# Optimization experiments

Measured on AMD Instinct MI355X. Metric: run time of the kernel, lower is better.

Reference implementation:

```python
import jax, jax.numpy as jnp
import numpy as np

CODEBOOK_SIZE = 1024
CODEBOOK_DIM = 256
B, H, W = 32, 64, 64


def setup_inputs() -> dict:
    key = jax.random.key(0)
    kx, kc = jax.random.split(key)
    x = jax.random.normal(kx, (B, CODEBOOK_DIM, H, W), dtype=jnp.float32)
    # nn.init.uniform_(weight, -1/K, 1/K)
    bound = 1.0 / CODEBOOK_SIZE
    codebook = jax.random.uniform(kc, (CODEBOOK_SIZE, CODEBOOK_DIM),
                                  minval=-bound, maxval=bound, dtype=jnp.float32)
    return {"x": x, "codebook": codebook}


def reference(x, codebook):
    b, c, h, w = x.shape
    z_e = jnp.transpose(x, (0, 2, 3, 1))            # [b,h,w,c]
    z_flat = z_e.reshape(-1, c)                      # [N,c]
    # squared L2 distances: ||z||^2 + ||e||^2 - 2 z.e
    dists = (jnp.sum(z_flat * z_flat, axis=1, keepdims=True)
             + jnp.sum(codebook * codebook, axis=1)
             - 2.0 * jnp.matmul(z_flat, codebook.T))  # [N,K]
    idx = jnp.argmin(dists, axis=1)                  # [N] int
    z_q = codebook[idx].reshape(b, h, w, c)          # [b,h,w,c]
    # commitment + codebook loss (both detach patterns)
    loss = (jnp.mean((jax.lax.stop_gradient(z_e) - z_q) ** 2)
            + jnp.mean((jax.lax.stop_gradient(z_q) - z_e) ** 2))
    # straight-through estimator
    z_q_st = z_e + jax.lax.stop_gradient(z_q - z_e)
    z_q_out = jnp.transpose(z_q_st, (0, 3, 1, 2))    # [b,c,h,w]
    return z_q_out, idx, loss
```

## Files before the change

kernel.cpp:

```cpp
#include <hip/hip_runtime.h>


typedef __attribute__((ext_vector_type(8))) short short8;
typedef __attribute__((ext_vector_type(4))) float f32x4;
typedef unsigned long long u64;

#define IDX_OFF   33554432u
#define LOSS_OFF  33685504u
#define IMG_BYTE  67108864u
#define CAND_BYTE 68157440u
#define ENRM_BYTE 69206016u

__device__ __forceinline__ unsigned short f2bf(float f) {
  unsigned u = __float_as_uint(f);
  unsigned r = (u + 0x7FFFu + ((u >> 16) & 1u)) >> 16;
  return (unsigned short)r;
}

#define COMB(r) __fadd_rn(__fadd_rn(__fadd_rn(r[0], r[1]), __fadd_rn(r[2], r[3])), \
                          __fadd_rn(__fadd_rn(r[4], r[5]), __fadd_rn(r[6], r[7])))

extern "C" __global__ __launch_bounds__(256) void vq_r11_k0(const float* __restrict__ cb,
                                                            unsigned char* __restrict__ img,
                                                            float* __restrict__ outf) {
  unsigned tid = blockIdx.x * 256u + threadIdx.x;
  unsigned code = tid >> 7, dp = tid & 127u;
  const float* p = cb + (size_t)code * 256u + dp * 2u;
  unsigned u = ((unsigned)f2bf(p[1]) << 16) | (unsigned)f2bf(p[0]);
  unsigned kc = code >> 6, n = (code >> 4) & 3, c16 = code & 15;
  unsigned ks = dp >> 4, g = (dp >> 2) & 3, j = dp & 3;
  unsigned byte = kc * 32768u + (n * 8u + ks) * 1024u + (g * 16u + c16) * 16u + j * 4u;
  *(unsigned*)(img + byte) = u;
  if (tid == 0) outf[LOSS_OFF] = 0.0f;
}

extern "C" __global__ __launch_bounds__(256) void vq_r11_k0b(const float* __restrict__ cb,
                                                             float* __restrict__ enrm) {
#pragma clang fp contract(off)
  int c = blockIdx.x * 256 + threadIdx.x;
  const float* e = cb + (size_t)c * 256u;
  float h[2];
#pragma unroll
  for (int half = 0; half < 2; ++half) {
    float r[8];
#pragma unroll
    for (int j = 0; j < 8; ++j) {
      float v = e[half * 128 + j];
      r[j] = __fmul_rn(v, v);
    }
    for (int i = 8; i < 128; i += 8) {
#pragma unroll
      for (int j = 0; j < 8; ++j) {
        float v = e[half * 128 + i + j];
        r[j] = __fadd_rn(r[j], __fmul_rn(v, v));
      }
    }
    h[half] = COMB(r);
  }
  enrm[c] = __fadd_rn(h[0], h[1]);
}

__device__ __forceinline__ void issue_frags(const unsigned char* gsrc, char* ldst) {
#pragma unroll
  for (int ks = 0; ks < 8; ++ks)
    __builtin_amdgcn_global_load_lds(
        (const __attribute__((address_space(1))) unsigned int*)(gsrc + ks * 1024),
        (__attribute__((address_space(3))) unsigned int*)(ldst + ks * 1024),
        16, 0, 0);
}

extern "C" __global__ __launch_bounds__(256, 2) void vq_r11_k1(const float* __restrict__ x,
                                                               const unsigned char* __restrict__ img,
                                                               u64* __restrict__ cand4) {
  __shared__ __attribute__((aligned(16))) char lds[65536];
  const int t = threadIdx.x;
  const int bid = blockIdx.x;
  const int lane = t & 63;
  const int w = t >> 6;
  const int g = lane >> 4, c16 = lane & 15;

  const size_t xbase = (size_t)(bid >> 4) * 1048576u + (size_t)(bid & 15) * 256u;

  short8 a[4][8];
  for (int q = 0; q < 4; ++q) {
#pragma unroll 4
    for (int s = 0; s < 8; ++s) {
      int flat = s * 256 + t;
      int pt4 = flat & 15;
      int dp = flat >> 4;
      const float* px = x + xbase + (size_t)(2 * dp) * 4096u + (unsigned)(q * 64 + pt4 * 4);
      float4 fa = *(const float4*)px;
      float4 fb = *(const float4*)(px + 4096);
      const float* fap = (const float*)&fa;
      const float* fbp = (const float*)&fb;
#pragma unroll
      for (int k = 0; k < 4; ++k) {
        unsigned u = ((unsigned)f2bf(fbp[k]) << 16) | (unsigned)f2bf(fap[k]);
        int r = pt4 * 4 + k;
        *(unsigned*)(lds + r * 512 + ((dp * 4) ^ ((r & 31) << 2))) = u;
      }
    }
    __syncthreads();
    if (w == q) {
#pragma unroll
      for (int m = 0; m < 4; ++m) {
        const int r = m * 16 + c16;
        const int rsw = (r & 31) << 2;
#pragma unroll
        for (int ks = 0; ks < 8; ++ks) {
          union { unsigned q4[4]; short8 s8; } uu;
#pragma unroll
          for (int jj = 0; jj < 4; ++jj)
            uu.q4[jj] = *(const unsigned*)(lds + r * 512 + (((ks * 16 + g * 4 + jj) * 4) ^ rsw));
          a[m][ks] = uu.s8;
        }
      }
    }
    __syncthreads();
  }

  float t1[16], t2[16];
#pragma unroll
  for (int s = 0; s < 16; ++s) { t1[s] = -__builtin_inff(); t2[s] = -__builtin_inff(); }

  char* ldsW = lds + w * 16384;
  const unsigned char* gW = img + (unsigned)(lane * 16);

  issue_frags(gW, ldsW);

  for (int s = 0; s < 64; ++s) {
    char* cur = ldsW + (s & 1) * 8192;
    asm volatile("s_waitcnt lgkmcnt(0)" ::: "memory");
    if (s < 63) {
      issue_frags(gW + (unsigned)((s + 1) * 8192), ldsW + ((s + 1) & 1) * 8192);
      asm volatile("s_waitcnt vmcnt(8)" ::: "memory");
    } else {
      asm volatile("s_waitcnt vmcnt(0)" ::: "memory");
    }

    f32x4 acc0 = (f32x4){0.f, 0.f, 0.f, 0.f};
    f32x4 acc1 = (f32x4){0.f, 0.f, 0.f, 0.f};
    f32x4 acc2 = (f32x4){0.f, 0.f, 0.f, 0.f};
    f32x4 acc3 = (f32x4){0.f, 0.f, 0.f, 0.f};
#pragma unroll
    for (int ks = 0; ks < 8; ++ks) {
      short8 b = *(const short8*)(cur + ks * 1024 + lane * 16);
      acc0 = __builtin_amdgcn_mfma_f32_16x16x32_bf16(a[0][ks], b, acc0, 0, 0, 0);
      acc1 = __builtin_amdgcn_mfma_f32_16x16x32_bf16(a[1][ks], b, acc1, 0, 0, 0);
      acc2 = __builtin_amdgcn_mfma_f32_16x16x32_bf16(a[2][ks], b, acc2, 0, 0, 0);
      acc3 = __builtin_amdgcn_mfma_f32_16x16x32_bf16(a[3][ks], b, acc3, 0, 0, 0);
    }
    const unsigned code = (unsigned)(s * 16 + c16);
#define SCRN(v, sl) { float kf = __uint_as_float((__float_as_uint(v) & 0xFFFFFC00u) | code); \
                      t2[sl] = __builtin_amdgcn_fmed3f(kf, t1[sl], t2[sl]); \
                      t1[sl] = fmaxf(t1[sl], kf); }
#pragma unroll
    for (int i = 0; i < 4; ++i) {
      SCRN(acc0[i], i);
      SCRN(acc1[i], 4 + i);
      SCRN(acc2[i], 8 + i);
      SCRN(acc3[i], 12 + i);
    }
#undef SCRN
  }

  __syncthreads();
  float* kk = (float*)lds;
#pragma unroll
  for (int m = 0; m < 4; ++m)
#pragma unroll
    for (int i = 0; i < 4; ++i) {
      int pt = w * 64 + m * 16 + g * 4 + i;
      kk[pt * 32 + c16 * 2] = t1[m * 4 + i];
      kk[pt * 32 + c16 * 2 + 1] = t2[m * 4 + i];
    }
  __syncthreads();

  {
    float f1 = -__builtin_inff(), f2v = f1, f3 = f1, f4 = f1;
#pragma unroll
    for (int j = 0; j < 32; ++j) {
      float v = kk[t * 32 + ((j + t) & 31)];
      float b1 = fminf(f1, v);   f1 = fmaxf(f1, v);
      float b2 = fminf(f2v, b1); f2v = fmaxf(f2v, b1);
      float b3 = fminf(f3, b2);  f3 = fmaxf(f3, b2);
      f4 = fmaxf(f4, b3);
    }
    u64 pk = (u64)(__float_as_uint(f1) & 1023u)
           | ((u64)(__float_as_uint(f2v) & 1023u) << 16)
           | ((u64)(__float_as_uint(f3) & 1023u) << 32)
           | ((u64)(__float_as_uint(f4) & 1023u) << 48);
    cand4[(size_t)bid * 256u + (unsigned)t] = pk;
  }
}

extern "C" __global__ __launch_bounds__(256) void vq_r11_k2(const float* __restrict__ x,
                                                            const float* __restrict__ cb,
                                                            const u64* __restrict__ cand4,
                                                            const float* __restrict__ enrm,
                                                            float* __restrict__ outf) {
#pragma clang fp contract(off)
  __shared__ double dts[4][64];
  __shared__ float s1s[64];
  const int t = threadIdx.x;
  const int pl = t & 63;
  const int c = t >> 6;
  const unsigned p = blockIdx.x * 64u + (unsigned)pl;

  const u64 pk = cand4[p];
  const int code = (int)((pk >> (16 * c)) & 1023u);

  const size_t xoff = ((size_t)(p >> 12)) * 1048576u + (size_t)(p & 4095u);
  const float* e = cb + (size_t)code * 256u;

  double da = 0.0, db = 0.0;
  float hs1[2];
#pragma unroll
  for (int half = 0; half < 2; ++half) {
    float r[8];
#pragma unroll 2
    for (int i = 0; i < 128; i += 8) {
      const int dbase = half * 128 + i;
      float q[8], xv[8];
      *(float4*)(q) = *(const float4*)(e + dbase);
      *(float4*)(q + 4) = *(const float4*)(e + dbase + 4);
#pragma unroll
      for (int j = 0; j < 8; ++j) xv[j] = x[xoff + (size_t)(dbase + j) * 4096u];
#pragma unroll
      for (int j = 0; j < 8; ++j) {
        r[j] = (i == 0) ? __fmul_rn(xv[j], xv[j])
                        : __fadd_rn(r[j], __fmul_rn(xv[j], xv[j]));
        if (j & 1) db = fma((double)xv[j], (double)q[j], db);
        else       da = fma((double)xv[j], (double)q[j], da);
      }
    }
    hs1[half] = COMB(r);
  }
  dts[c][pl] = da + db;
  if (c == 0) s1s[pl] = __fadd_rn(hs1[0], hs1[1]);
  __syncthreads();

  if (t < 64) {
    const float s1v = s1s[pl];
    float bestd = __builtin_inff();
    int besti = 0x7FFFFFFF;
#pragma unroll
    for (int cc = 0; cc < 4; ++cc) {
      const int ccode = (int)((pk >> (16 * cc)) & 1023u);
      float dd = __fsub_rn(__fadd_rn(s1v, enrm[ccode]),
                           __fmul_rn(2.0f, (float)dts[cc][pl]));
      if (dd < bestd || (dd == bestd && ccode < besti)) { bestd = dd; besti = ccode; }
    }
    outf[IDX_OFF + p] = (float)besti;

    float sum = bestd;
#pragma unroll
    for (int off = 32; off > 0; off >>= 1) sum += __shfl_down(sum, off);
    if (pl == 0) atomicAdd(outf + LOSS_OFF, sum);
  }
}

extern "C" __global__ void vq_r11_k4(float* __restrict__ outf) {
  if (threadIdx.x == 0 && blockIdx.x == 0)
    outf[LOSS_OFF] = 2.0f * (outf[LOSS_OFF] / 33554432.0f);
}

extern "C" __global__ __launch_bounds__(256) void vq_r11_k3(const float* __restrict__ cb,
                                                            float* __restrict__ outf) {
  __shared__ float rows[32 * 257];
  const int t = threadIdx.x;
  const unsigned p0 = blockIdx.x * 32u;
  const unsigned b = p0 >> 12, hw0 = p0 & 4095u;
  const float* idxf = outf + IDX_OFF;
  for (int i = 0; i < 32; ++i) {
    int row = ((int)idxf[p0 + (unsigned)i]) & 1023;
    rows[i * 257 + t] = cb[(size_t)row * 256u + (unsigned)t];
  }
  __syncthreads();
  const int q = t & 7, cgrp = t >> 3;
  float* obase = outf + (size_t)b * 1048576u + hw0 + (unsigned)(q * 4);
#pragma unroll
  for (int cc = 0; cc < 8; ++cc) {
    int c = cgrp * 8 + cc;
    float4 v;
    v.x = rows[(q * 4 + 0) * 257 + c];
    v.y = rows[(q * 4 + 1) * 257 + c];
    v.z = rows[(q * 4 + 2) * 257 + c];
    v.w = rows[(q * 4 + 3) * 257 + c];
    *(float4*)(obase + (size_t)c * 4096u) = v;
  }
}

extern "C" void kernel_launch(void* const* d_in, const int* in_sizes, int n_in,
                              void* d_out, int out_size, void* d_ws, size_t ws_size,
                              hipStream_t stream) {
  const float* x = (const float*)d_in[0];
  const float* cb = (const float*)d_in[1];
  float* outf = (float*)d_out;
  unsigned char* img = (unsigned char*)d_out + IMG_BYTE;
  u64* cand4 = (u64*)((unsigned char*)d_out + CAND_BYTE);
  float* enrm = (float*)((unsigned char*)d_out + ENRM_BYTE);
  (void)in_sizes; (void)n_in; (void)out_size; (void)d_ws; (void)ws_size;

  vq_r11_k0<<<512, 256, 0, stream>>>(cb, img, outf);
  vq_r11_k0b<<<4, 256, 0, stream>>>(cb, enrm);
  vq_r11_k1<<<512, 256, 0, stream>>>(x, img, cand4);
  vq_r11_k2<<<2048, 256, 0, stream>>>(x, cb, cand4, enrm, outf);
  vq_r11_k4<<<1, 64, 0, stream>>>(outf);
  vq_r11_k3<<<4096, 256, 0, stream>>>(cb, outf);
}
```

Before: 214.2 us.

## Load codebook fragments directly into registers and ping-pong accumulators across steps

The distance kernel stops staging codebook fragments through LDS with global_load_lds double buffering. It now loads the B fragments straight from global memory into registers. The codebook image layout is simplified to one contiguous 8 KB block per 16-code step, and the main loop is unrolled by two with alternating accumulator sets so the top-2 screening of one step overlaps the MFMAs and loads of the next. LDS shrinks to 32 KB, used only by the A-tile transpose and the final merge. The trade-off is higher register pressure and exposed global-load latency instead of LDS staging.

```diff
diff --git a/kernel.cpp b/kernel.cpp
--- a/kernel.cpp
+++ b/kernel.cpp
@@ -20,21 +20,21 @@
 #define COMB(r) __fadd_rn(__fadd_rn(__fadd_rn(r[0], r[1]), __fadd_rn(r[2], r[3])), \
                           __fadd_rn(__fadd_rn(r[4], r[5]), __fadd_rn(r[6], r[7])))
 
-extern "C" __global__ __launch_bounds__(256) void vq_r11_k0(const float* __restrict__ cb,
+extern "C" __global__ __launch_bounds__(256) void vq_r12_k0(const float* __restrict__ cb,
                                                             unsigned char* __restrict__ img,
                                                             float* __restrict__ outf) {
   unsigned tid = blockIdx.x * 256u + threadIdx.x;
   unsigned code = tid >> 7, dp = tid & 127u;
   const float* p = cb + (size_t)code * 256u + dp * 2u;
   unsigned u = ((unsigned)f2bf(p[1]) << 16) | (unsigned)f2bf(p[0]);
-  unsigned kc = code >> 6, n = (code >> 4) & 3, c16 = code & 15;
+  unsigned s = code >> 4, c16 = code & 15;
   unsigned ks = dp >> 4, g = (dp >> 2) & 3, j = dp & 3;
-  unsigned byte = kc * 32768u + (n * 8u + ks) * 1024u + (g * 16u + c16) * 16u + j * 4u;
+  unsigned byte = (s * 8u + ks) * 1024u + (g * 16u + c16) * 16u + j * 4u;
   *(unsigned*)(img + byte) = u;
   if (tid == 0) outf[LOSS_OFF] = 0.0f;
 }
 
-extern "C" __global__ __launch_bounds__(256) void vq_r11_k0b(const float* __restrict__ cb,
+extern "C" __global__ __launch_bounds__(256) void vq_r12_k0b(const float* __restrict__ cb,
                                                              float* __restrict__ enrm) {
 #pragma clang fp contract(off)
   int c = blockIdx.x * 256 + threadIdx.x;
@@ -60,19 +60,23 @@
   enrm[c] = __fadd_rn(h[0], h[1]);
 }
 
-__device__ __forceinline__ void issue_frags(const unsigned char* gsrc, char* ldst) {
-#pragma unroll
-  for (int ks = 0; ks < 8; ++ks)
-    __builtin_amdgcn_global_load_lds(
-        (const __attribute__((address_space(1))) unsigned int*)(gsrc + ks * 1024),
-        (__attribute__((address_space(3))) unsigned int*)(ldst + ks * 1024),
-        16, 0, 0);
-}
-
-extern "C" __global__ __launch_bounds__(256, 2) void vq_r11_k1(const float* __restrict__ x,
+__device__ __forceinline__ void screen16(const f32x4* acc, unsigned code,
+                                         float* t1, float* t2) {
+#pragma unroll
+  for (int m = 0; m < 4; ++m)
+#pragma unroll
+    for (int i = 0; i < 4; ++i) {
+      float kf = __uint_as_float((__float_as_uint(acc[m][i]) & 0xFFFFFC00u) | code);
+      int s = m * 4 + i;
+      t2[s] = __builtin_amdgcn_fmed3f(kf, t1[s], t2[s]);
+      t1[s] = fmaxf(t1[s], kf);
+    }
+}
+
+extern "C" __global__ __launch_bounds__(256, 2) void vq_r12_k1(const float* __restrict__ x,
                                                                const unsigned char* __restrict__ img,
                                                                u64* __restrict__ cand4) {
-  __shared__ __attribute__((aligned(16))) char lds[65536];
+  __shared__ __attribute__((aligned(16))) char lds[32768];
   const int t = threadIdx.x;
   const int bid = blockIdx.x;
   const int lane = t & 63;
@@ -123,48 +127,51 @@
 #pragma unroll
   for (int s = 0; s < 16; ++s) { t1[s] = -__builtin_inff(); t2[s] = -__builtin_inff(); }
 
-  char* ldsW = lds + w * 16384;
   const unsigned char* gW = img + (unsigned)(lane * 16);
-
-  issue_frags(gW, ldsW);
-
-  for (int s = 0; s < 64; ++s) {
-    char* cur = ldsW + (s & 1) * 8192;
-    asm volatile("s_waitcnt lgkmcnt(0)" ::: "memory");
-    if (s < 63) {
-      issue_frags(gW + (unsigned)((s + 1) * 8192), ldsW + ((s + 1) & 1) * 8192);
-      asm volatile("s_waitcnt vmcnt(8)" ::: "memory");
-    } else {
-      asm volatile("s_waitcnt vmcnt(0)" ::: "memory");
-    }
-
-    f32x4 acc0 = (f32x4){0.f, 0.f, 0.f, 0.f};
-    f32x4 acc1 = (f32x4){0.f, 0.f, 0.f, 0.f};
-    f32x4 acc2 = (f32x4){0.f, 0.f, 0.f, 0.f};
-    f32x4 acc3 = (f32x4){0.f, 0.f, 0.f, 0.f};
+  short8 bf[8];
+  f32x4 accA[4], accB[4];
+
+#pragma unroll
+  for (int ks = 0; ks < 8; ++ks)
+    bf[ks] = *(const short8*)(gW + ks * 1024);
+
+  for (int s2 = 0; s2 < 32; ++s2) {
+    const int s = s2 * 2;
+#pragma unroll
+    for (int i = 0; i < 4; ++i) accA[i] = (f32x4){0.f, 0.f, 0.f, 0.f};
 #pragma unroll
     for (int ks = 0; ks < 8; ++ks) {
-      short8 b = *(const short8*)(cur + ks * 1024 + lane * 16);
-      acc0 = __builtin_amdgcn_mfma_f32_16x16x32_bf16(a[0][ks], b, acc0, 0, 0, 0);
-      acc1 = __builtin_amdgcn_mfma_f32_16x16x32_bf16(a[1][ks], b, acc1, 0, 0, 0);
-      acc2 = __builtin_amdgcn_mfma_f32_16x16x32_bf16(a[2][ks], b, acc2, 0, 0, 0);
-      acc3 = __builtin_amdgcn_mfma_f32_16x16x32_bf16(a[3][ks], b, acc3, 0, 0, 0);
-    }
-    const unsigned code = (unsigned)(s * 16 + c16);
-#define SCRN(v, sl) { float kf = __uint_as_float((__float_as_uint(v) & 0xFFFFFC00u) | code); \
-                      t2[sl] = __builtin_amdgcn_fmed3f(kf, t1[sl], t2[sl]); \
-                      t1[sl] = fmaxf(t1[sl], kf); }
-#pragma unroll
-    for (int i = 0; i < 4; ++i) {
-      SCRN(acc0[i], i);
-      SCRN(acc1[i], 4 + i);
-      SCRN(acc2[i], 8 + i);
-      SCRN(acc3[i], 12 + i);
-    }
-#undef SCRN
-  }
-
-  __syncthreads();
+      accA[0] = __builtin_amdgcn_mfma_f32_16x16x32_bf16(a[0][ks], bf[ks], accA[0], 0, 0, 0);
+      accA[1] = __builtin_amdgcn_mfma_f32_16x16x32_bf16(a[1][ks], bf[ks], accA[1], 0, 0, 0);
+      accA[2] = __builtin_amdgcn_mfma_f32_16x16x32_bf16(a[2][ks], bf[ks], accA[2], 0, 0, 0);
+      accA[3] = __builtin_amdgcn_mfma_f32_16x16x32_bf16(a[3][ks], bf[ks], accA[3], 0, 0, 0);
+    }
+    {
+      const unsigned char* g1 = gW + (unsigned)((s + 1) * 8192);
+#pragma unroll
+      for (int ks = 0; ks < 8; ++ks) bf[ks] = *(const short8*)(g1 + ks * 1024);
+    }
+    if (s2 != 0)
+      screen16(accB, (unsigned)((s - 1) * 16 + c16), t1, t2);
+
+#pragma unroll
+    for (int i = 0; i < 4; ++i) accB[i] = (f32x4){0.f, 0.f, 0.f, 0.f};
+#pragma unroll
+    for (int ks = 0; ks < 8; ++ks) {
+      accB[0] = __builtin_amdgcn_mfma_f32_16x16x32_bf16(a[0][ks], bf[ks], accB[0], 0, 0, 0);
+      accB[1] = __builtin_amdgcn_mfma_f32_16x16x32_bf16(a[1][ks], bf[ks], accB[1], 0, 0, 0);
+      accB[2] = __builtin_amdgcn_mfma_f32_16x16x32_bf16(a[2][ks], bf[ks], accB[2], 0, 0, 0);
+      accB[3] = __builtin_amdgcn_mfma_f32_16x16x32_bf16(a[3][ks], bf[ks], accB[3], 0, 0, 0);
+    }
+    if (s2 != 31) {
+      const unsigned char* g2 = gW + (unsigned)((s + 2) * 8192);
+#pragma unroll
+      for (int ks = 0; ks < 8; ++ks) bf[ks] = *(const short8*)(g2 + ks * 1024);
+    }
+    screen16(accA, (unsigned)(s * 16 + c16), t1, t2);
+  }
+  screen16(accB, (unsigned)(63 * 16 + c16), t1, t2);
+
   float* kk = (float*)lds;
 #pragma unroll
   for (int m = 0; m < 4; ++m)
@@ -194,7 +201,7 @@
   }
 }
 
-extern "C" __global__ __launch_bounds__(256) void vq_r11_k2(const float* __restrict__ x,
+extern "C" __global__ __launch_bounds__(256) void vq_r12_k2(const float* __restrict__ x,
                                                             const float* __restrict__ cb,
                                                             const u64* __restrict__ cand4,
                                                             const float* __restrict__ enrm,
@@ -260,12 +267,12 @@
   }
 }
 
-extern "C" __global__ void vq_r11_k4(float* __restrict__ outf) {
+extern "C" __global__ void vq_r12_k4(float* __restrict__ outf) {
   if (threadIdx.x == 0 && blockIdx.x == 0)
     outf[LOSS_OFF] = 2.0f * (outf[LOSS_OFF] / 33554432.0f);
 }
 
-extern "C" __global__ __launch_bounds__(256) void vq_r11_k3(const float* __restrict__ cb,
+extern "C" __global__ __launch_bounds__(256) void vq_r12_k3(const float* __restrict__ cb,
                                                             float* __restrict__ outf) {
   __shared__ float rows[32 * 257];
   const int t = threadIdx.x;
@@ -302,10 +309,10 @@
   float* enrm = (float*)((unsigned char*)d_out + ENRM_BYTE);
   (void)in_sizes; (void)n_in; (void)out_size; (void)d_ws; (void)ws_size;
 
-  vq_r11_k0<<<512, 256, 0, stream>>>(cb, img, outf);
-  vq_r11_k0b<<<4, 256, 0, stream>>>(cb, enrm);
-  vq_r11_k1<<<512, 256, 0, stream>>>(x, img, cand4);
-  vq_r11_k2<<<2048, 256, 0, stream>>>(x, cb, cand4, enrm, outf);
-  vq_r11_k4<<<1, 64, 0, stream>>>(outf);
-  vq_r11_k3<<<4096, 256, 0, stream>>>(cb, outf);
-}
+  vq_r12_k0<<<512, 256, 0, stream>>>(cb, img, outf);
+  vq_r12_k0b<<<4, 256, 0, stream>>>(cb, enrm);
+  vq_r12_k1<<<512, 256, 0, stream>>>(x, img, cand4);
+  vq_r12_k2<<<2048, 256, 0, stream>>>(x, cb, cand4, enrm, outf);
+  vq_r12_k4<<<1, 64, 0, stream>>>(outf);
+  vq_r12_k3<<<4096, 256, 0, stream>>>(cb, outf);
+}
```

New measurement: 212.3 us. Within noise of the previous version (-0.9%).

## Halve points per block, load codebook fragments directly to registers, raise occupancy

Applied to the files above, without the earlier changes.

The distance kernel now handles 128 points per block instead of 256, and each wave holds 32 query rows instead of 64. The global→LDS double-buffered prefetch of codebook tiles is replaced by direct global loads into registers, with the codebook image relaid out linearly by code group. LDS drops to 32KB, launch bounds allow 3 blocks per CU, and the grid doubles to 1024. The intent is more occupancy and less LDS traffic, at the cost of reading the codebook twice as often in total and having less MFMA work per loaded B fragment.

```diff
diff --git a/kernel.cpp b/kernel.cpp
--- a/kernel.cpp
+++ b/kernel.cpp
@@ -20,21 +20,21 @@
 #define COMB(r) __fadd_rn(__fadd_rn(__fadd_rn(r[0], r[1]), __fadd_rn(r[2], r[3])), \
                           __fadd_rn(__fadd_rn(r[4], r[5]), __fadd_rn(r[6], r[7])))
 
-extern "C" __global__ __launch_bounds__(256) void vq_r11_k0(const float* __restrict__ cb,
+extern "C" __global__ __launch_bounds__(256) void vq_r13_k0(const float* __restrict__ cb,
                                                             unsigned char* __restrict__ img,
                                                             float* __restrict__ outf) {
   unsigned tid = blockIdx.x * 256u + threadIdx.x;
   unsigned code = tid >> 7, dp = tid & 127u;
   const float* p = cb + (size_t)code * 256u + dp * 2u;
   unsigned u = ((unsigned)f2bf(p[1]) << 16) | (unsigned)f2bf(p[0]);
-  unsigned kc = code >> 6, n = (code >> 4) & 3, c16 = code & 15;
+  unsigned s = code >> 4, c16 = code & 15;
   unsigned ks = dp >> 4, g = (dp >> 2) & 3, j = dp & 3;
-  unsigned byte = kc * 32768u + (n * 8u + ks) * 1024u + (g * 16u + c16) * 16u + j * 4u;
+  unsigned byte = (s * 8u + ks) * 1024u + (g * 16u + c16) * 16u + j * 4u;
   *(unsigned*)(img + byte) = u;
   if (tid == 0) outf[LOSS_OFF] = 0.0f;
 }
 
-extern "C" __global__ __launch_bounds__(256) void vq_r11_k0b(const float* __restrict__ cb,
+extern "C" __global__ __launch_bounds__(256) void vq_r13_k0b(const float* __restrict__ cb,
                                                              float* __restrict__ enrm) {
 #pragma clang fp contract(off)
   int c = blockIdx.x * 256 + threadIdx.x;
@@ -60,35 +60,26 @@
   enrm[c] = __fadd_rn(h[0], h[1]);
 }
 
-__device__ __forceinline__ void issue_frags(const unsigned char* gsrc, char* ldst) {
-#pragma unroll
-  for (int ks = 0; ks < 8; ++ks)
-    __builtin_amdgcn_global_load_lds(
-        (const __attribute__((address_space(1))) unsigned int*)(gsrc + ks * 1024),
-        (__attribute__((address_space(3))) unsigned int*)(ldst + ks * 1024),
-        16, 0, 0);
-}
-
-extern "C" __global__ __launch_bounds__(256, 2) void vq_r11_k1(const float* __restrict__ x,
+extern "C" __global__ __launch_bounds__(256, 3) void vq_r13_k1(const float* __restrict__ x,
                                                                const unsigned char* __restrict__ img,
                                                                u64* __restrict__ cand4) {
-  __shared__ __attribute__((aligned(16))) char lds[65536];
+  __shared__ __attribute__((aligned(16))) char lds[32768];
   const int t = threadIdx.x;
   const int bid = blockIdx.x;
   const int lane = t & 63;
   const int w = t >> 6;
   const int g = lane >> 4, c16 = lane & 15;
 
-  const size_t xbase = (size_t)(bid >> 4) * 1048576u + (size_t)(bid & 15) * 256u;
-
-  short8 a[4][8];
-  for (int q = 0; q < 4; ++q) {
+  const size_t xbase = (size_t)(bid >> 5) * 1048576u + (size_t)(bid & 31) * 128u;
+
+  short8 a[2][8];
+  for (int h = 0; h < 2; ++h) {
 #pragma unroll 4
-    for (int s = 0; s < 8; ++s) {
-      int flat = s * 256 + t;
+    for (int it = 0; it < 8; ++it) {
+      int flat = it * 256 + t;
       int pt4 = flat & 15;
       int dp = flat >> 4;
-      const float* px = x + xbase + (size_t)(2 * dp) * 4096u + (unsigned)(q * 64 + pt4 * 4);
+      const float* px = x + xbase + (size_t)(2 * dp) * 4096u + (unsigned)(h * 64 + pt4 * 4);
       float4 fa = *(const float4*)px;
       float4 fb = *(const float4*)(px + 4096);
       const float* fap = (const float*)&fa;
@@ -101,10 +92,10 @@
       }
     }
     __syncthreads();
-    if (w == q) {
-#pragma unroll
-      for (int m = 0; m < 4; ++m) {
-        const int r = m * 16 + c16;
+    if ((w >> 1) == h) {
+#pragma unroll
+      for (int m = 0; m < 2; ++m) {
+        const int r = (w & 1) * 32 + m * 16 + c16;
         const int rsw = (r & 31) << 2;
 #pragma unroll
         for (int ks = 0; ks < 8; ++ks) {
@@ -119,36 +110,23 @@
     __syncthreads();
   }
 
-  float t1[16], t2[16];
-#pragma unroll
-  for (int s = 0; s < 16; ++s) { t1[s] = -__builtin_inff(); t2[s] = -__builtin_inff(); }
-
-  char* ldsW = lds + w * 16384;
+  float t1[8], t2[8];
+#pragma unroll
+  for (int s = 0; s < 8; ++s) { t1[s] = -__builtin_inff(); t2[s] = -__builtin_inff(); }
+
   const unsigned char* gW = img + (unsigned)(lane * 16);
-
-  issue_frags(gW, ldsW);
-
   for (int s = 0; s < 64; ++s) {
-    char* cur = ldsW + (s & 1) * 8192;
-    asm volatile("s_waitcnt lgkmcnt(0)" ::: "memory");
-    if (s < 63) {
-      issue_frags(gW + (unsigned)((s + 1) * 8192), ldsW + ((s + 1) & 1) * 8192);
-      asm volatile("s_waitcnt vmcnt(8)" ::: "memory");
-    } else {
-      asm volatile("s_waitcnt vmcnt(0)" ::: "memory");
-    }
-
+    const unsigned char* gs = gW + (unsigned)(s * 8192);
+    short8 bf[8];
+#pragma unroll
+    for (int ks = 0; ks < 8; ++ks)
+      bf[ks] = *(const short8*)(gs + ks * 1024);
     f32x4 acc0 = (f32x4){0.f, 0.f, 0.f, 0.f};
     f32x4 acc1 = (f32x4){0.f, 0.f, 0.f, 0.f};
-    f32x4 acc2 = (f32x4){0.f, 0.f, 0.f, 0.f};
-    f32x4 acc3 = (f32x4){0.f, 0.f, 0.f, 0.f};
 #pragma unroll
     for (int ks = 0; ks < 8; ++ks) {
-      short8 b = *(const short8*)(cur + ks * 1024 + lane * 16);
-      acc0 = __builtin_amdgcn_mfma_f32_16x16x32_bf16(a[0][ks], b, acc0, 0, 0, 0);
-      acc1 = __builtin_amdgcn_mfma_f32_16x16x32_bf16(a[1][ks], b, acc1, 0, 0, 0);
-      acc2 = __builtin_amdgcn_mfma_f32_16x16x32_bf16(a[2][ks], b, acc2, 0, 0, 0);
-      acc3 = __builtin_amdgcn_mfma_f32_16x16x32_bf16(a[3][ks], b, acc3, 0, 0, 0);
+      acc0 = __builtin_amdgcn_mfma_f32_16x16x32_bf16(a[0][ks], bf[ks], acc0, 0, 0, 0);
+      acc1 = __builtin_amdgcn_mfma_f32_16x16x32_bf16(a[1][ks], bf[ks], acc1, 0, 0, 0);
     }
     const unsigned code = (unsigned)(s * 16 + c16);
 #define SCRN(v, sl) { float kf = __uint_as_float((__float_as_uint(v) & 0xFFFFFC00u) | code); \
@@ -158,8 +136,6 @@
     for (int i = 0; i < 4; ++i) {
       SCRN(acc0[i], i);
       SCRN(acc1[i], 4 + i);
-      SCRN(acc2[i], 8 + i);
-      SCRN(acc3[i], 12 + i);
     }
 #undef SCRN
   }
@@ -167,16 +143,16 @@
   __syncthreads();
   float* kk = (float*)lds;
 #pragma unroll
-  for (int m = 0; m < 4; ++m)
+  for (int m = 0; m < 2; ++m)
 #pragma unroll
     for (int i = 0; i < 4; ++i) {
-      int pt = w * 64 + m * 16 + g * 4 + i;
+      int pt = w * 32 + m * 16 + g * 4 + i;
       kk[pt * 32 + c16 * 2] = t1[m * 4 + i];
       kk[pt * 32 + c16 * 2 + 1] = t2[m * 4 + i];
     }
   __syncthreads();
 
-  {
+  if (t < 128) {
     float f1 = -__builtin_inff(), f2v = f1, f3 = f1, f4 = f1;
 #pragma unroll
     for (int j = 0; j < 32; ++j) {
@@ -190,11 +166,11 @@
            | ((u64)(__float_as_uint(f2v) & 1023u) << 16)
            | ((u64)(__float_as_uint(f3) & 1023u) << 32)
            | ((u64)(__float_as_uint(f4) & 1023u) << 48);
-    cand4[(size_t)bid * 256u + (unsigned)t] = pk;
-  }
-}
-
-extern "C" __global__ __launch_bounds__(256) void vq_r11_k2(const float* __restrict__ x,
+    cand4[(size_t)bid * 128u + (unsigned)t] = pk;
+  }
+}
+
+extern "C" __global__ __launch_bounds__(256) void vq_r13_k2(const float* __restrict__ x,
                                                             const float* __restrict__ cb,
                                                             const u64* __restrict__ cand4,
                                                             const float* __restrict__ enrm,
@@ -260,12 +236,12 @@
   }
 }
 
-extern "C" __global__ void vq_r11_k4(float* __restrict__ outf) {
+extern "C" __global__ void vq_r13_k4(float* __restrict__ outf) {
   if (threadIdx.x == 0 && blockIdx.x == 0)
     outf[LOSS_OFF] = 2.0f * (outf[LOSS_OFF] / 33554432.0f);
 }
 
-extern "C" __global__ __launch_bounds__(256) void vq_r11_k3(const float* __restrict__ cb,
+extern "C" __global__ __launch_bounds__(256) void vq_r13_k3(const float* __restrict__ cb,
                                                             float* __restrict__ outf) {
   __shared__ float rows[32 * 257];
   const int t = threadIdx.x;
@@ -302,10 +278,10 @@
   float* enrm = (float*)((unsigned char*)d_out + ENRM_BYTE);
   (void)in_sizes; (void)n_in; (void)out_size; (void)d_ws; (void)ws_size;
 
-  vq_r11_k0<<<512, 256, 0, stream>>>(cb, img, outf);
-  vq_r11_k0b<<<4, 256, 0, stream>>>(cb, enrm);
-  vq_r11_k1<<<512, 256, 0, stream>>>(x, img, cand4);
-  vq_r11_k2<<<2048, 256, 0, stream>>>(x, cb, cand4, enrm, outf);
-  vq_r11_k4<<<1, 64, 0, stream>>>(outf);
-  vq_r11_k3<<<4096, 256, 0, stream>>>(cb, outf);
-}
+  vq_r13_k0<<<512, 256, 0, stream>>>(cb, img, outf);
+  vq_r13_k0b<<<4, 256, 0, stream>>>(cb, enrm);
+  vq_r13_k1<<<1024, 256, 0, stream>>>(x, img, cand4);
+  vq_r13_k2<<<2048, 256, 0, stream>>>(x, cb, cand4, enrm, outf);
+  vq_r13_k4<<<1, 64, 0, stream>>>(outf);
+  vq_r13_k3<<<4096, 256, 0, stream>>>(cb, outf);
+}
```

Result: slower. 223.2 us (+4.2%).

## Load codebook fragments directly to registers and fold small kernels together

Applied to the files above, without the earlier changes.

The main scoring kernel no longer stages codebook B-fragments through double-buffered LDS with async global_load_lds. It reads them straight from global memory into registers each step, raises wave priority around the MFMA block, and halves the LDS allocation, which may allow more occupancy. The codebook-norm kernel is merged into the bf16 image-packing kernel, and the loss-finalize kernel is folded into the gather kernel, removing two launches. The image layout is simplified to match the new per-step read pattern. The trade-off is that global load latency is no longer overlapped by an explicit prefetch. The loss finalization in block 0 of the gather kernel relies on stream ordering after the accumulating kernel.

```diff
diff --git a/kernel.cpp b/kernel.cpp
--- a/kernel.cpp
+++ b/kernel.cpp
@@ -20,59 +20,49 @@
 #define COMB(r) __fadd_rn(__fadd_rn(__fadd_rn(r[0], r[1]), __fadd_rn(r[2], r[3])), \
                           __fadd_rn(__fadd_rn(r[4], r[5]), __fadd_rn(r[6], r[7])))
 
-extern "C" __global__ __launch_bounds__(256) void vq_r11_k0(const float* __restrict__ cb,
+extern "C" __global__ __launch_bounds__(256) void vq_r14_k0(const float* __restrict__ cb,
                                                             unsigned char* __restrict__ img,
+                                                            float* __restrict__ enrm,
                                                             float* __restrict__ outf) {
+#pragma clang fp contract(off)
   unsigned tid = blockIdx.x * 256u + threadIdx.x;
   unsigned code = tid >> 7, dp = tid & 127u;
   const float* p = cb + (size_t)code * 256u + dp * 2u;
   unsigned u = ((unsigned)f2bf(p[1]) << 16) | (unsigned)f2bf(p[0]);
-  unsigned kc = code >> 6, n = (code >> 4) & 3, c16 = code & 15;
+  unsigned s = code >> 4, c16 = code & 15;
   unsigned ks = dp >> 4, g = (dp >> 2) & 3, j = dp & 3;
-  unsigned byte = kc * 32768u + (n * 8u + ks) * 1024u + (g * 16u + c16) * 16u + j * 4u;
+  unsigned byte = (s * 8u + ks) * 1024u + (g * 16u + c16) * 16u + j * 4u;
   *(unsigned*)(img + byte) = u;
   if (tid == 0) outf[LOSS_OFF] = 0.0f;
-}
-
-extern "C" __global__ __launch_bounds__(256) void vq_r11_k0b(const float* __restrict__ cb,
-                                                             float* __restrict__ enrm) {
-#pragma clang fp contract(off)
-  int c = blockIdx.x * 256 + threadIdx.x;
-  const float* e = cb + (size_t)c * 256u;
-  float h[2];
-#pragma unroll
-  for (int half = 0; half < 2; ++half) {
-    float r[8];
-#pragma unroll
-    for (int j = 0; j < 8; ++j) {
-      float v = e[half * 128 + j];
-      r[j] = __fmul_rn(v, v);
-    }
-    for (int i = 8; i < 128; i += 8) {
-#pragma unroll
-      for (int j = 0; j < 8; ++j) {
-        float v = e[half * 128 + i + j];
-        r[j] = __fadd_rn(r[j], __fmul_rn(v, v));
-      }
-    }
-    h[half] = COMB(r);
-  }
-  enrm[c] = __fadd_rn(h[0], h[1]);
-}
-
-__device__ __forceinline__ void issue_frags(const unsigned char* gsrc, char* ldst) {
-#pragma unroll
-  for (int ks = 0; ks < 8; ++ks)
-    __builtin_amdgcn_global_load_lds(
-        (const __attribute__((address_space(1))) unsigned int*)(gsrc + ks * 1024),
-        (__attribute__((address_space(3))) unsigned int*)(ldst + ks * 1024),
-        16, 0, 0);
-}
-
-extern "C" __global__ __launch_bounds__(256, 2) void vq_r11_k1(const float* __restrict__ x,
+
+  if (tid < 1024u) {
+    const float* e = cb + (size_t)tid * 256u;
+    float h[2];
+#pragma unroll
+    for (int half = 0; half < 2; ++half) {
+      float r[8];
+#pragma unroll
+      for (int jj = 0; jj < 8; ++jj) {
+        float v = e[half * 128 + jj];
+        r[jj] = __fmul_rn(v, v);
+      }
+      for (int i = 8; i < 128; i += 8) {
+#pragma unroll
+        for (int jj = 0; jj < 8; ++jj) {
+          float v = e[half * 128 + i + jj];
+          r[jj] = __fadd_rn(r[jj], __fmul_rn(v, v));
+        }
+      }
+      h[half] = COMB(r);
+    }
+    enrm[tid] = __fadd_rn(h[0], h[1]);
+  }
+}
+
+extern "C" __global__ __launch_bounds__(256, 2) void vq_r14_k1(const float* __restrict__ x,
                                                                const unsigned char* __restrict__ img,
                                                                u64* __restrict__ cand4) {
-  __shared__ __attribute__((aligned(16))) char lds[65536];
+  __shared__ __attribute__((aligned(16))) char lds[32768];
   const int t = threadIdx.x;
   const int bid = blockIdx.x;
   const int lane = t & 63;
@@ -123,33 +113,26 @@
 #pragma unroll
   for (int s = 0; s < 16; ++s) { t1[s] = -__builtin_inff(); t2[s] = -__builtin_inff(); }
 
-  char* ldsW = lds + w * 16384;
   const unsigned char* gW = img + (unsigned)(lane * 16);
-
-  issue_frags(gW, ldsW);
-
   for (int s = 0; s < 64; ++s) {
-    char* cur = ldsW + (s & 1) * 8192;
-    asm volatile("s_waitcnt lgkmcnt(0)" ::: "memory");
-    if (s < 63) {
-      issue_frags(gW + (unsigned)((s + 1) * 8192), ldsW + ((s + 1) & 1) * 8192);
-      asm volatile("s_waitcnt vmcnt(8)" ::: "memory");
-    } else {
-      asm volatile("s_waitcnt vmcnt(0)" ::: "memory");
-    }
-
+    const unsigned char* gs = gW + (unsigned)(s * 8192);
+    short8 bf[8];
+#pragma unroll
+    for (int ks = 0; ks < 8; ++ks)
+      bf[ks] = *(const short8*)(gs + ks * 1024);
     f32x4 acc0 = (f32x4){0.f, 0.f, 0.f, 0.f};
     f32x4 acc1 = (f32x4){0.f, 0.f, 0.f, 0.f};
     f32x4 acc2 = (f32x4){0.f, 0.f, 0.f, 0.f};
     f32x4 acc3 = (f32x4){0.f, 0.f, 0.f, 0.f};
+    __builtin_amdgcn_s_setprio(1);
 #pragma unroll
     for (int ks = 0; ks < 8; ++ks) {
-      short8 b = *(const short8*)(cur + ks * 1024 + lane * 16);
-      acc0 = __builtin_amdgcn_mfma_f32_16x16x32_bf16(a[0][ks], b, acc0, 0, 0, 0);
-      acc1 = __builtin_amdgcn_mfma_f32_16x16x32_bf16(a[1][ks], b, acc1, 0, 0, 0);
-      acc2 = __builtin_amdgcn_mfma_f32_16x16x32_bf16(a[2][ks], b, acc2, 0, 0, 0);
-      acc3 = __builtin_amdgcn_mfma_f32_16x16x32_bf16(a[3][ks], b, acc3, 0, 0, 0);
-    }
+      acc0 = __builtin_amdgcn_mfma_f32_16x16x32_bf16(a[0][ks], bf[ks], acc0, 0, 0, 0);
+      acc1 = __builtin_amdgcn_mfma_f32_16x16x32_bf16(a[1][ks], bf[ks], acc1, 0, 0, 0);
+      acc2 = __builtin_amdgcn_mfma_f32_16x16x32_bf16(a[2][ks], bf[ks], acc2, 0, 0, 0);
+      acc3 = __builtin_amdgcn_mfma_f32_16x16x32_bf16(a[3][ks], bf[ks], acc3, 0, 0, 0);
+    }
+    __builtin_amdgcn_s_setprio(0);
     const unsigned code = (unsigned)(s * 16 + c16);
 #define SCRN(v, sl) { float kf = __uint_as_float((__float_as_uint(v) & 0xFFFFFC00u) | code); \
                       t2[sl] = __builtin_amdgcn_fmed3f(kf, t1[sl], t2[sl]); \
@@ -194,7 +177,7 @@
   }
 }
 
-extern "C" __global__ __launch_bounds__(256) void vq_r11_k2(const float* __restrict__ x,
+extern "C" __global__ __launch_bounds__(256) void vq_r14_k2(const float* __restrict__ x,
                                                             const float* __restrict__ cb,
                                                             const u64* __restrict__ cand4,
                                                             const float* __restrict__ enrm,
@@ -260,15 +243,12 @@
   }
 }
 
-extern "C" __global__ void vq_r11_k4(float* __restrict__ outf) {
-  if (threadIdx.x == 0 && blockIdx.x == 0)
-    outf[LOSS_OFF] = 2.0f * (outf[LOSS_OFF] / 33554432.0f);
-}
-
-extern "C" __global__ __launch_bounds__(256) void vq_r11_k3(const float* __restrict__ cb,
+extern "C" __global__ __launch_bounds__(256) void vq_r14_k3(const float* __restrict__ cb,
                                                             float* __restrict__ outf) {
   __shared__ float rows[32 * 257];
   const int t = threadIdx.x;
+  if (blockIdx.x == 0 && t == 0)
+    outf[LOSS_OFF] = 2.0f * (outf[LOSS_OFF] / 33554432.0f);
   const unsigned p0 = blockIdx.x * 32u;
   const unsigned b = p0 >> 12, hw0 = p0 & 4095u;
   const float* idxf = outf + IDX_OFF;
@@ -302,10 +282,8 @@
   float* enrm = (float*)((unsigned char*)d_out + ENRM_BYTE);
   (void)in_sizes; (void)n_in; (void)out_size; (void)d_ws; (void)ws_size;
 
-  vq_r11_k0<<<512, 256, 0, stream>>>(cb, img, outf);
-  vq_r11_k0b<<<4, 256, 0, stream>>>(cb, enrm);
-  vq_r11_k1<<<512, 256, 0, stream>>>(x, img, cand4);
-  vq_r11_k2<<<2048, 256, 0, stream>>>(x, cb, cand4, enrm, outf);
-  vq_r11_k4<<<1, 64, 0, stream>>>(outf);
-  vq_r11_k3<<<4096, 256, 0, stream>>>(cb, outf);
-}
+  vq_r14_k0<<<512, 256, 0, stream>>>(cb, img, enrm, outf);
+  vq_r14_k1<<<512, 256, 0, stream>>>(x, img, cand4);
+  vq_r14_k2<<<2048, 256, 0, stream>>>(x, cb, cand4, enrm, outf);
+  vq_r14_k3<<<4096, 256, 0, stream>>>(cb, outf);
+}
```

After: 195.8 us. 1.09x faster.
